# Kernel optimization log

Hardware: AMD Instinct MI355X
Metric: run time of the kernel (lower is better)

## Reference

```python
import jax, jax.numpy as jnp
import numpy as np

B, N, FIN, FOUT = 2, 8192, 128, 64


def _mlp2(x, W1, b1, W2, b2):
    # two pointwise (kernel-size-1 Conv1D) layers, each with ReLU
    h = jax.nn.relu(jnp.einsum('bnf,fo->bno', x, W1) + b1)
    return jax.nn.relu(jnp.einsum('bnf,fo->bno', h, W2) + b2)


def setup_inputs() -> dict:
    key = jax.random.key(0)
    ks = jax.random.split(key, 9)
    s_in = 1.0 / np.sqrt(FIN)
    s_h = 1.0 / np.sqrt(FOUT)
    return {
        'feature': jax.random.normal(ks[0], (B, N, FIN), jnp.float32),
        'x_weight': jax.random.uniform(ks[1], (B, N, N), jnp.float32),
        'W1_1': jax.random.normal(ks[2], (FIN, FOUT), jnp.float32) * s_in,
        'b1_1': jnp.zeros((FOUT,), jnp.float32),
        'W1_2': jax.random.normal(ks[3], (FOUT, FOUT), jnp.float32) * s_h,
        'b1_2': jnp.zeros((FOUT,), jnp.float32),
        'W2_1': jax.random.normal(ks[4], (FIN, FOUT), jnp.float32) * s_in,
        'b2_1': jnp.zeros((FOUT,), jnp.float32),
        'W2_2': jax.random.normal(ks[5], (FOUT, FOUT), jnp.float32) * s_h,
        'b2_2': jnp.zeros((FOUT,), jnp.float32),
        'W3_1': jax.random.normal(ks[6], (FIN, FOUT), jnp.float32) * s_in,
        'b3_1': jnp.zeros((FOUT,), jnp.float32),
        'W3_2': jax.random.normal(ks[7], (FOUT, FOUT), jnp.float32) * s_h,
        'b3_2': jnp.zeros((FOUT,), jnp.float32),
    }


def reference(feature, x_weight, W1_1, b1_1, W1_2, b1_2,
              W2_1, b2_1, W2_2, b2_2, W3_1, b3_1, W3_2, b3_2):
    q = _mlp2(feature, W1_1, b1_1, W1_2, b1_2)  # [B, N, Fout]
    k = _mlp2(feature, W2_1, b2_1, W2_2, b2_2)  # [B, N, Fout]
    v = _mlp2(feature, W3_1, b3_1, W3_2, b3_2)  # [B, N, Fout]
    logits = jnp.einsum('bnf,bmf->bnm', q, k) * x_weight  # [B, N, N]
    coefs = jax.nn.softmax(jax.nn.relu(logits), axis=-1)
    return jax.nn.relu(jnp.einsum('bnm,bmf->bnf', coefs, v))  # [B, N, Fout]
```

## Files before the change

### kernel.cpp

```cpp
#include <hip/hip_runtime.h>

#define NB   8192
#define BATCH 2
#define FIN  128
#define FO   64
#define SPLIT 4
#define NSUP (NB / SPLIT / 64)

typedef _Float16 f16;
typedef _Float16 f16x4 __attribute__((ext_vector_type(4)));
typedef _Float16 f16x8 __attribute__((ext_vector_type(8)));
typedef float    f32x4 __attribute__((ext_vector_type(4)));

__device__ __forceinline__ f32x4 mfma16(f16x4 a, f16x4 b, f32x4 c) {
    return __builtin_amdgcn_mfma_f32_16x16x16f16(a, b, c, 0, 0, 0);
}
__device__ __forceinline__ f32x4 mfma32(f16x8 a, f16x8 b, f32x4 c) {
    return __builtin_amdgcn_mfma_f32_16x16x32_f16(a, b, c, 0, 0, 0);
}

#define GLOAD_LDS16(gsrc, ldst)                                                   \
    __builtin_amdgcn_global_load_lds(                                             \
        (const __attribute__((address_space(1))) unsigned int*)(gsrc),            \
        (__attribute__((address_space(3))) unsigned int*)(ldst), 16, 0, 0)

__global__ void k_prep(const float* __restrict__ W11, const float* __restrict__ W21,
                       const float* __restrict__ W31, const float* __restrict__ W12,
                       const float* __restrict__ W22, const float* __restrict__ W32,
                       f16* __restrict__ W1t, f16* __restrict__ W2t) {
    int gid = blockIdx.x * 256 + threadIdx.x;
    if (gid < 3 * FIN * FO) {
        int m = gid >> 13, rem = gid & (FIN * FO - 1);
        int k = rem >> 6, c = rem & 63;
        const float* src = m == 0 ? W11 : (m == 1 ? W21 : W31);
        W1t[m * FIN * FO + c * FIN + k] = (f16)src[k * FO + c];
    } else {
        int idx = gid - 3 * FIN * FO;
        if (idx < 3 * FO * FO) {
            int m = idx >> 12, rem = idx & (FO * FO - 1);
            int k = rem >> 6, c = rem & 63;
            const float* src = m == 0 ? W12 : (m == 1 ? W22 : W32);
            W2t[m * FO * FO + c * FO + k] = (f16)src[k * FO + c];
        }
    }
}

__global__ __launch_bounds__(256) void k_qkv(
    const float* __restrict__ feat,
    const float* __restrict__ b1q, const float* __restrict__ b2q,
    const float* __restrict__ b1k, const float* __restrict__ b2k,
    const float* __restrict__ b1v, const float* __restrict__ b2v,
    const f16* __restrict__ W1t, const f16* __restrict__ W2t,
    f16* __restrict__ qbuf, f16* __restrict__ kbuf, f16* __restrict__ vtbuf) {
    __shared__ f16 Hs[4][16][68];
    const int tid = threadIdx.x;
    const int l15 = tid & 15, quad = (tid >> 4) & 3, w = tid >> 6;
    const int m = blockIdx.x >> 8;
    const int row0 = (blockIdx.x & 255) * 64;
    const int rbase = row0 + w * 16;
    const int bb = row0 >> 13;
    const int n0 = row0 & (NB - 1);

    f16x4 xf[8];
    const float* xp = feat + (size_t)(rbase + l15) * FIN + quad * 4;
#pragma unroll
    for (int kk = 0; kk < 8; ++kk) {
        float4 t = *(const float4*)(xp + kk * 16);
        f16x4 h; h[0] = (f16)t.x; h[1] = (f16)t.y; h[2] = (f16)t.z; h[3] = (f16)t.w;
        xf[kk] = h;
    }

    const float* b1 = m == 0 ? b1q : (m == 1 ? b1k : b1v);
    const float* b2 = m == 0 ? b2q : (m == 1 ? b2k : b2v);
    const f16* w1 = W1t + m * FIN * FO;
    const f16* w2 = W2t + m * FO * FO;

    f32x4 hacc[4] = {};
#pragma unroll
    for (int kk = 0; kk < 8; ++kk) {
#pragma unroll
        for (int nt = 0; nt < 4; ++nt) {
            f16x4 bf = *(const f16x4*)(w1 + (nt * 16 + l15) * FIN + kk * 16 + quad * 4);
            hacc[nt] = mfma16(xf[kk], bf, hacc[nt]);
        }
    }
#pragma unroll
    for (int nt = 0; nt < 4; ++nt) {
        float bv = b1[nt * 16 + l15];
#pragma unroll
        for (int r = 0; r < 4; ++r) {
            float v = hacc[nt][r] + bv;
            Hs[w][quad * 4 + r][nt * 16 + l15] = (f16)(v > 0.f ? v : 0.f);
        }
    }
    __syncthreads();

    f32x4 oacc[4] = {};
#pragma unroll
    for (int kk = 0; kk < 4; ++kk) {
        f16x4 af = *(const f16x4*)(&Hs[w][l15][kk * 16 + quad * 4]);
#pragma unroll
        for (int nt = 0; nt < 4; ++nt) {
            f16x4 bf = *(const f16x4*)(w2 + (nt * 16 + l15) * FO + kk * 16 + quad * 4);
            oacc[nt] = mfma16(af, bf, oacc[nt]);
        }
    }
#pragma unroll
    for (int nt = 0; nt < 4; ++nt) {
        float bv = b2[nt * 16 + l15];
        int col = nt * 16 + l15;
#pragma unroll
        for (int r = 0; r < 4; ++r) {
            float v = oacc[nt][r] + bv;
            f16 hv = (f16)(v > 0.f ? v : 0.f);
            int rl = w * 16 + quad * 4 + r;
            if (m == 0)      qbuf[(size_t)(row0 + rl) * FO + col] = hv;
            else if (m == 1) kbuf[(size_t)(row0 + rl) * FO + col] = hv;
            else             vtbuf[((size_t)bb * FO + col) * NB + n0 + rl] = hv;
        }
    }
}

__global__ __launch_bounds__(256, 4) void k_attn(
    const float* __restrict__ xw,
    const f16* __restrict__ qbuf, const f16* __restrict__ kbuf,
    const f16* __restrict__ vtbuf,
    float* __restrict__ Obuf, float* __restrict__ mbuf, float* __restrict__ lbuf) {
    __shared__ __align__(16) f16 Ks[2][64][64];
    __shared__ __align__(16) f16 Vs[2][64][64];

    const int tid = threadIdx.x;
    const int lane = tid & 63;
    const int l15 = tid & 15, quad = (tid >> 4) & 3, w = tid >> 6;
    const int bid = blockIdx.x;
    const int split = bid & (SPLIT - 1);
    const int rest = bid / SPLIT;
    const int qblk = rest & 127;
    const int bb = rest >> 7;
    const int qn = qblk * 64 + w * 16;
    const int kv0 = split * (NB / SPLIT);

    const f16* qp = qbuf + (size_t)(bb * NB + qn + l15) * FO + quad * 8;
    f16x8 qf[2];
#pragma unroll
    for (int kk = 0; kk < 2; ++kk) qf[kk] = *(const f16x8*)(qp + kk * 32);

    const int cl_a = (w * 2 + 0) * 64 + lane;
    const int cl_b = (w * 2 + 1) * 64 + lane;
    const int row_a = cl_a >> 3, sw_a = (cl_a & 7) ^ (row_a & 7);
    const int row_b = cl_b >> 3, sw_b = (cl_b & 7) ^ (row_b & 7);
    const f16* kb = kbuf + (size_t)(bb * NB + kv0) * FO;
    const f16* vb = vtbuf + (size_t)bb * FO * NB + kv0;

    const float* xwp = xw + (size_t)(bb * NB + qn + l15) * NB + kv0 + quad * 4;

    auto STAGE = [&](int buf, int sp) {
        f16* kd = &Ks[buf][0][0];
        f16* vd = &Vs[buf][0][0];
        GLOAD_LDS16(kb + (size_t)(sp * 64 + row_a) * FO + sw_a * 8, kd + (w * 2 + 0) * 512);
        GLOAD_LDS16(kb + (size_t)(sp * 64 + row_b) * FO + sw_b * 8, kd + (w * 2 + 1) * 512);
        GLOAD_LDS16(vb + (size_t)row_a * NB + sp * 64 + sw_a * 8,   vd + (w * 2 + 0) * 512);
        GLOAD_LDS16(vb + (size_t)row_b * NB + sp * 64 + sw_b * 8,   vd + (w * 2 + 1) * 512);
    };

    f32x4 oacc[4] = {};
    float m_run = 0.f, l_run = 0.f;

    STAGE(0, 0);
    f32x4 xwn[4];
#pragma unroll
    for (int st = 0; st < 4; ++st) xwn[st] = *(const f32x4*)(xwp + st * 16);
    __syncthreads();

    const int sxor = (l15 & 7) << 4;

    for (int sp = 0; sp < NSUP; ++sp) {
        const int cur = sp & 1;
        if (sp + 1 < NSUP) STAGE(cur ^ 1, sp + 1);

        f32x4 xwc[4];
#pragma unroll
        for (int st = 0; st < 4; ++st) xwc[st] = xwn[st];
        int spn = (sp + 1 < NSUP) ? sp + 1 : sp;
#pragma unroll
        for (int st = 0; st < 4; ++st) xwn[st] = *(const f32x4*)(xwp + spn * 64 + st * 16);

        const char* kbase = (const char*)&Ks[cur][0][0];
        const char* vbase = (const char*)&Vs[cur][0][0];

        f32x4 s[4];
#pragma unroll
        for (int st = 0; st < 4; ++st) {
            f32x4 acc = {};
#pragma unroll
            for (int kk = 0; kk < 2; ++kk) {
                f16x8 kf = *(const f16x8*)(kbase + (st * 16 + l15) * 128 +
                                           ((kk * 64 + quad * 16) ^ sxor));
                acc = mfma32(kf, qf[kk], acc);
            }
            s[st] = acc;
        }
        float tm = 0.f;
#pragma unroll
        for (int st = 0; st < 4; ++st)
#pragma unroll
            for (int r = 0; r < 4; ++r) {
                float v = s[st][r] * xwc[st][r];
                v = v > 0.f ? v : 0.f;
                s[st][r] = v;
                tm = fmaxf(tm, v);
            }
        tm = fmaxf(tm, __shfl_xor(tm, 16));
        tm = fmaxf(tm, __shfl_xor(tm, 32));
        float m_new = fmaxf(m_run, tm);
        float alpha = __expf(m_run - m_new);
        l_run *= alpha;
#pragma unroll
        for (int dt = 0; dt < 4; ++dt)
#pragma unroll
            for (int r = 0; r < 4; ++r) oacc[dt][r] *= alpha;
        m_run = m_new;

        f16x4 pf[4];
#pragma unroll
        for (int st = 0; st < 4; ++st) {
            float p0 = __expf(s[st][0] - m_new);
            float p1 = __expf(s[st][1] - m_new);
            float p2 = __expf(s[st][2] - m_new);
            float p3 = __expf(s[st][3] - m_new);
            l_run += (p0 + p1) + (p2 + p3);
            f16x4 h; h[0] = (f16)p0; h[1] = (f16)p1; h[2] = (f16)p2; h[3] = (f16)p3;
            pf[st] = h;
        }
#pragma unroll
        for (int st = 0; st < 4; ++st)
#pragma unroll
            for (int dt = 0; dt < 4; ++dt) {
                f16x4 vf = *(const f16x4*)(vbase + (dt * 16 + l15) * 128 +
                                           ((st * 32 + quad * 8) ^ sxor));
                oacc[dt] = mfma16(vf, pf[st], oacc[dt]);
            }

        __syncthreads();
    }

    l_run += __shfl_xor(l_run, 16);
    l_run += __shfl_xor(l_run, 32);

    size_t orow = ((size_t)split * BATCH + bb) * NB + qn + l15;
#pragma unroll
    for (int dt = 0; dt < 4; ++dt)
        *(f32x4*)(Obuf + orow * FO + dt * 16 + quad * 4) = oacc[dt];
    if (quad == 0) { mbuf[orow] = m_run; lbuf[orow] = l_run; }
}

__global__ void k_comb(const float* __restrict__ Obuf, const float* __restrict__ mbuf,
                       const float* __restrict__ lbuf, float* __restrict__ out) {
    int gid = blockIdx.x * 256 + threadIdx.x;
    int bn = gid >> 6;
    const int S = BATCH * NB;
    float m0 = mbuf[bn], m1 = mbuf[S + bn], m2 = mbuf[2 * S + bn], m3 = mbuf[3 * S + bn];
    float M = fmaxf(fmaxf(m0, m1), fmaxf(m2, m3));
    float e0 = __expf(m0 - M), e1 = __expf(m1 - M), e2 = __expf(m2 - M), e3 = __expf(m3 - M);
    float L = lbuf[bn] * e0 + lbuf[S + bn] * e1 + lbuf[2 * S + bn] * e2 + lbuf[3 * S + bn] * e3;
    const int ST = S * FO;
    float o = Obuf[gid] * e0 + Obuf[gid + ST] * e1 + Obuf[gid + 2 * ST] * e2 + Obuf[gid + 3 * ST] * e3;
    float v = o / L;
    out[gid] = v > 0.f ? v : 0.f;
}

extern "C" void kernel_launch(void* const* d_in, const int* in_sizes, int n_in,
                              void* d_out, int out_size, void* d_ws, size_t ws_size,
                              hipStream_t stream) {
    const float* feat = (const float*)d_in[0];
    const float* xw   = (const float*)d_in[1];
    const float* W11 = (const float*)d_in[2];  const float* b11 = (const float*)d_in[3];
    const float* W12 = (const float*)d_in[4];  const float* b12 = (const float*)d_in[5];
    const float* W21 = (const float*)d_in[6];  const float* b21 = (const float*)d_in[7];
    const float* W22 = (const float*)d_in[8];  const float* b22 = (const float*)d_in[9];
    const float* W31 = (const float*)d_in[10]; const float* b31 = (const float*)d_in[11];
    const float* W32 = (const float*)d_in[12]; const float* b32 = (const float*)d_in[13];

    char* ws = (char*)d_ws;
    f16*   W1t  = (f16*)(ws);
    f16*   W2t  = (f16*)(ws + 49152);
    f16*   qbuf = (f16*)(ws + 73728);
    f16*   kbuf = (f16*)(ws + 73728 + 2097152);
    f16*   vtbuf= (f16*)(ws + 73728 + 4194304);
    float* Obuf = (float*)(ws + 73728 + 6291456);
    float* mbuf = (float*)(ws + 73728 + 23068672);
    float* lbuf = (float*)(ws + 73728 + 23330816);

    k_prep<<<144, 256, 0, stream>>>(W11, W21, W31, W12, W22, W32, W1t, W2t);
    k_qkv<<<768, 256, 0, stream>>>(feat, b11, b12, b21, b22, b31, b32,
                                   W1t, W2t, qbuf, kbuf, vtbuf);
    k_attn<<<BATCH * 128 * SPLIT, 256, 0, stream>>>(xw, qbuf, kbuf, vtbuf,
                                                    Obuf, mbuf, lbuf);
    k_comb<<<4096, 256, 0, stream>>>(Obuf, mbuf, lbuf, (float*)d_out);
}
```

Baseline: 769.3 us.

## Double-buffer x_weight prefetch two tiles ahead with manual waitcnt and barriers

The attention loop now keeps two register buffers of x_weight and issues the load for tile sp+2 after the PV MFMAs. It replaces __syncthreads with explicit vmcnt waits plus s_barrier, so only the LDS stage loads are drained while the x_weight prefetch stays in flight. MFMA sections are wrapped in s_setprio to favour matrix issue. Separately, the V projection now transposes through shared memory so vtbuf is written with 16-byte vector stores instead of scattered 2-byte writes. The hand-counted vmcnt(4) relies on exact load ordering, and the extra x_weight registers may reduce occupancy.

```diff
diff --git a/kernel.cpp b/kernel.cpp
--- a/kernel.cpp
+++ b/kernel.cpp
@@ -53,6 +53,7 @@
     const f16* __restrict__ W1t, const f16* __restrict__ W2t,
     f16* __restrict__ qbuf, f16* __restrict__ kbuf, f16* __restrict__ vtbuf) {
     __shared__ f16 Hs[4][16][68];
+    __shared__ f16 Vt[64][72];
     const int tid = threadIdx.x;
     const int l15 = tid & 15, quad = (tid >> 4) & 3, w = tid >> 6;
     const int m = blockIdx.x >> 8;
@@ -105,18 +106,38 @@
             oacc[nt] = mfma16(af, bf, oacc[nt]);
         }
     }
-#pragma unroll
-    for (int nt = 0; nt < 4; ++nt) {
-        float bv = b2[nt * 16 + l15];
-        int col = nt * 16 + l15;
-#pragma unroll
-        for (int r = 0; r < 4; ++r) {
-            float v = oacc[nt][r] + bv;
-            f16 hv = (f16)(v > 0.f ? v : 0.f);
-            int rl = w * 16 + quad * 4 + r;
-            if (m == 0)      qbuf[(size_t)(row0 + rl) * FO + col] = hv;
-            else if (m == 1) kbuf[(size_t)(row0 + rl) * FO + col] = hv;
-            else             vtbuf[((size_t)bb * FO + col) * NB + n0 + rl] = hv;
+    if (m == 2) {
+#pragma unroll
+        for (int nt = 0; nt < 4; ++nt) {
+            float bv = b2[nt * 16 + l15];
+            f16x4 h;
+#pragma unroll
+            for (int r = 0; r < 4; ++r) {
+                float v = oacc[nt][r] + bv;
+                h[r] = (f16)(v > 0.f ? v : 0.f);
+            }
+            *(f16x4*)&Vt[nt * 16 + l15][w * 16 + quad * 4] = h;
+        }
+        __syncthreads();
+        int c = tid >> 2, part = tid & 3;
+        f16x8 v0 = *(const f16x8*)&Vt[c][part * 16];
+        f16x8 v1 = *(const f16x8*)&Vt[c][part * 16 + 8];
+        f16* dst = vtbuf + ((size_t)bb * FO + c) * NB + n0 + part * 16;
+        *(f16x8*)dst = v0;
+        *(f16x8*)(dst + 8) = v1;
+    } else {
+#pragma unroll
+        for (int nt = 0; nt < 4; ++nt) {
+            float bv = b2[nt * 16 + l15];
+            int col = nt * 16 + l15;
+#pragma unroll
+            for (int r = 0; r < 4; ++r) {
+                float v = oacc[nt][r] + bv;
+                f16 hv = (f16)(v > 0.f ? v : 0.f);
+                int rl = w * 16 + quad * 4 + r;
+                if (m == 0) qbuf[(size_t)(row0 + rl) * FO + col] = hv;
+                else        kbuf[(size_t)(row0 + rl) * FO + col] = hv;
+            }
         }
     }
 }
@@ -165,30 +186,28 @@
 
     f32x4 oacc[4] = {};
     float m_run = 0.f, l_run = 0.f;
-
+    const int sxor = (l15 & 7) << 4;
+
+    f32x4 xwA[4], xwB[4];
     STAGE(0, 0);
-    f32x4 xwn[4];
-#pragma unroll
-    for (int st = 0; st < 4; ++st) xwn[st] = *(const f32x4*)(xwp + st * 16);
-    __syncthreads();
-
-    const int sxor = (l15 & 7) << 4;
-
-    for (int sp = 0; sp < NSUP; ++sp) {
+#pragma unroll
+    for (int st = 0; st < 4; ++st) {
+        xwA[st] = *(const f32x4*)(xwp + st * 16);
+        xwB[st] = *(const f32x4*)(xwp + 64 + st * 16);
+    }
+    asm volatile("s_waitcnt vmcnt(0)" ::: "memory");
+    __builtin_amdgcn_s_barrier();
+    __builtin_amdgcn_sched_barrier(0);
+
+    auto ITER = [&](int sp, f32x4 (&xwc)[4]) {
         const int cur = sp & 1;
         if (sp + 1 < NSUP) STAGE(cur ^ 1, sp + 1);
 
-        f32x4 xwc[4];
-#pragma unroll
-        for (int st = 0; st < 4; ++st) xwc[st] = xwn[st];
-        int spn = (sp + 1 < NSUP) ? sp + 1 : sp;
-#pragma unroll
-        for (int st = 0; st < 4; ++st) xwn[st] = *(const f32x4*)(xwp + spn * 64 + st * 16);
-
         const char* kbase = (const char*)&Ks[cur][0][0];
         const char* vbase = (const char*)&Vs[cur][0][0];
 
         f32x4 s[4];
+        __builtin_amdgcn_s_setprio(1);
 #pragma unroll
         for (int st = 0; st < 4; ++st) {
             f32x4 acc = {};
@@ -200,6 +219,8 @@
             }
             s[st] = acc;
         }
+        __builtin_amdgcn_s_setprio(0);
+
         float tm = 0.f;
 #pragma unroll
         for (int st = 0; st < 4; ++st)
@@ -232,6 +253,7 @@
             f16x4 h; h[0] = (f16)p0; h[1] = (f16)p1; h[2] = (f16)p2; h[3] = (f16)p3;
             pf[st] = h;
         }
+        __builtin_amdgcn_s_setprio(1);
 #pragma unroll
         for (int st = 0; st < 4; ++st)
 #pragma unroll
@@ -240,8 +262,26 @@
                                            ((st * 32 + quad * 8) ^ sxor));
                 oacc[dt] = mfma16(vf, pf[st], oacc[dt]);
             }
-
-        __syncthreads();
+        __builtin_amdgcn_s_setprio(0);
+
+        asm volatile("" ::: "memory");
+        if (sp + 2 < NSUP) {
+#pragma unroll
+            for (int st = 0; st < 4; ++st)
+                xwc[st] = *(const f32x4*)(xwp + (sp + 2) * 64 + st * 16);
+            asm volatile("s_waitcnt vmcnt(4)" ::: "memory");
+        } else if (sp + 1 < NSUP) {
+            asm volatile("s_waitcnt vmcnt(0)" ::: "memory");
+        }
+        if (sp + 1 < NSUP) {
+            __builtin_amdgcn_s_barrier();
+            __builtin_amdgcn_sched_barrier(0);
+        }
+    };
+
+    for (int sp = 0; sp < NSUP; sp += 2) {
+        ITER(sp, xwA);
+        ITER(sp + 1, xwB);
     }
 
     l_run += __shfl_xor(l_run, 16);
```

New measurement: 763.7 us. About the same (-0.7%).
